# Performance work log

Measured on AMD Instinct MI355X. Metric: run time of the kernel, lower is better.

## Reference

```python
import jax, jax.numpy as jnp
import numpy as np

IN_FEATURES = 8192
OUT_FEATURES = 8192
POOL_K = 16
SCALE = 2.0


def setup_inputs() -> dict:
    key = jax.random.key(0)
    k1, k2, k3 = jax.random.split(key, 3)
    B = 4096
    x = jax.random.normal(k1, (B, IN_FEATURES), dtype=jnp.float32)
    # nn.Linear default init: U(-1/sqrt(fan_in), 1/sqrt(fan_in))
    bound = 1.0 / np.sqrt(IN_FEATURES)
    W = jax.random.uniform(k2, (OUT_FEATURES, IN_FEATURES), dtype=jnp.float32, minval=-bound, maxval=bound)
    b = jax.random.uniform(k3, (OUT_FEATURES,), dtype=jnp.float32, minval=-bound, maxval=bound)
    return {"x": x, "W": W, "b": b}


def reference(x, W, b):
    # GEMM: [B, C_out]
    y = jnp.dot(x, W.T) + b
    B, C = y.shape
    # AvgPool1d over feature dim, kernel=stride=POOL_K -> [B, C/POOL_K]
    pooled = y.reshape(B, C // POOL_K, POOL_K).mean(axis=-1)
    # GELU (tanh approximation) + scale, then row-wise max -> [B]
    v = jax.nn.gelu(pooled, approximate=True) * SCALE
    return jnp.max(v, axis=-1)
```

## Files before the change

kernel.cpp:

```cpp
#include <hip/hip_runtime.h>
#include <hip/hip_bf16.h>
#include <cmath>

#define M_DIM 4096
#define N_POOL 512
#define K_DIM 8192
#define KSPLIT 8
#define K_PER (K_DIM / KSPLIT)

typedef __bf16 bf16x8 __attribute__((ext_vector_type(8)));
typedef float floatx4 __attribute__((ext_vector_type(4)));
typedef unsigned short ushort8v __attribute__((ext_vector_type(8)));

__device__ __forceinline__ unsigned short f2bf(float f) {
  unsigned int u = __float_as_uint(f);
  return (unsigned short)((u + 0x7fffu + ((u >> 16) & 1u)) >> 16);
}

__global__ void convert_f32_bf16(const float4* __restrict__ src,
                                 ushort8v* __restrict__ dst, int n8) {
  int i = blockIdx.x * blockDim.x + threadIdx.x;
  int stride = gridDim.x * blockDim.x;
  for (; i < n8; i += stride) {
    float4 a = src[2 * i], b = src[2 * i + 1];
    ushort8v o;
    o[0] = f2bf(a.x); o[1] = f2bf(a.y); o[2] = f2bf(a.z); o[3] = f2bf(a.w);
    o[4] = f2bf(b.x); o[5] = f2bf(b.y); o[6] = f2bf(b.z); o[7] = f2bf(b.w);
    dst[i] = o;
  }
}

__global__ void wpool_kernel(const float* __restrict__ W,
                             unsigned short* __restrict__ Wp) {
  int g = blockIdx.x;
  const float* base = W + (size_t)g * 16 * K_DIM;
  ushort4* out = (ushort4*)(Wp + (size_t)g * K_DIM);
  for (int c4 = threadIdx.x; c4 < K_DIM / 4; c4 += blockDim.x) {
    float4 s = {0.f, 0.f, 0.f, 0.f};
#pragma unroll
    for (int j = 0; j < 16; ++j) {
      float4 v = ((const float4*)(base + (size_t)j * K_DIM))[c4];
      s.x += v.x; s.y += v.y; s.z += v.z; s.w += v.w;
    }
    ushort4 o;
    o.x = f2bf(s.x); o.y = f2bf(s.y); o.z = f2bf(s.z); o.w = f2bf(s.w);
    out[c4] = o;
  }
}

__global__ void bias_pool(const float* __restrict__ b, float* __restrict__ bpool) {
  int g = threadIdx.x;
  float s = 0.f;
  for (int i = 0; i < 16; ++i) s += b[g * 16 + i];
  bpool[g] = s;
}

__global__ __launch_bounds__(256) void gemm_splitk(
    const unsigned short* __restrict__ xb,
    const unsigned short* __restrict__ wp,
    float* __restrict__ part)
{
  __shared__ __align__(16) unsigned short As[128 * 64];
  __shared__ __align__(16) unsigned short Bs[128 * 64];

  const int tid = threadIdx.x;
  const int L = tid & 63;
  const int w = tid >> 6;
  const int wm = w & 1, wn = w >> 1;
  const int lane15 = L & 15, quad = L >> 4;

  const int bn = blockIdx.x, bm = blockIdx.y, kz = blockIdx.z;

  const int srow = w * 32 + (L >> 3);
  const int schunk = ((L & 7) ^ ((L >> 3) & 7)) * 8;
  const unsigned short* ga = xb + (size_t)(bm * 128 + srow) * K_DIM + kz * K_PER + schunk;
  const unsigned short* gb = wp + (size_t)(bn * 128 + srow) * K_DIM + kz * K_PER + schunk;
  unsigned short* lA = As + (w * 32) * 64;
  unsigned short* lB = Bs + (w * 32) * 64;

  floatx4 acc[4][4];
#pragma unroll
  for (int t = 0; t < 4; ++t)
#pragma unroll
    for (int u = 0; u < 4; ++u) acc[t][u] = (floatx4)0.f;

  const bf16x8* Av = (const bf16x8*)As;
  const bf16x8* Bv = (const bf16x8*)Bs;

  for (int kk = 0; kk < K_PER / 64; ++kk) {
#pragma unroll
    for (int i = 0; i < 4; ++i) {
      __builtin_amdgcn_global_load_lds(
          (const __attribute__((address_space(1))) void*)(ga + (size_t)(i * 8) * K_DIM),
          (__attribute__((address_space(3))) void*)(lA + i * 8 * 64), 16, 0, 0);
    }
#pragma unroll
    for (int i = 0; i < 4; ++i) {
      __builtin_amdgcn_global_load_lds(
          (const __attribute__((address_space(1))) void*)(gb + (size_t)(i * 8) * K_DIM),
          (__attribute__((address_space(3))) void*)(lB + i * 8 * 64), 16, 0, 0);
    }
    ga += 64; gb += 64;
    __syncthreads();

#pragma unroll
    for (int ks = 0; ks < 2; ++ks) {
      bf16x8 af[4], bfr[4];
#pragma unroll
      for (int t = 0; t < 4; ++t) {
        int r = wm * 64 + t * 16 + lane15;
        af[t] = Av[r * 8 + ((ks * 4 + quad) ^ (lane15 & 7))];
      }
#pragma unroll
      for (int u = 0; u < 4; ++u) {
        int r = wn * 64 + u * 16 + lane15;
        bfr[u] = Bv[r * 8 + ((ks * 4 + quad) ^ (lane15 & 7))];
      }
#pragma unroll
      for (int t = 0; t < 4; ++t)
#pragma unroll
        for (int u = 0; u < 4; ++u)
          acc[t][u] = __builtin_amdgcn_mfma_f32_16x16x32_bf16(af[t], bfr[u],
                                                              acc[t][u], 0, 0, 0);
    }
    __syncthreads();
  }

  float* cp = part + (size_t)kz * M_DIM * N_POOL;
  const int row_base = bm * 128 + wm * 64;
  const int col_base = bn * 128 + wn * 64;
#pragma unroll
  for (int t = 0; t < 4; ++t)
#pragma unroll
    for (int u = 0; u < 4; ++u) {
      int col = col_base + u * 16 + lane15;
#pragma unroll
      for (int r = 0; r < 4; ++r) {
        int row = row_base + t * 16 + quad * 4 + r;
        cp[(size_t)row * N_POOL + col] = acc[t][u][r];
      }
    }
}

__global__ void finalize(const float* __restrict__ part,
                         const float* __restrict__ bpool,
                         float* __restrict__ out) {
  int row = blockIdx.x;
  int lane = threadIdx.x;
  float mx = -INFINITY;
#pragma unroll
  for (int j = 0; j < 8; ++j) {
    int g = lane + j * 64;
    float s = bpool[g];
#pragma unroll
    for (int kz = 0; kz < KSPLIT; ++kz)
      s += part[(size_t)kz * M_DIM * N_POOL + (size_t)row * N_POOL + g];
    float p = s * 0.0625f;
    float t = tanhf(0.7978845608028654f * (p + 0.044715f * p * p * p));
    mx = fmaxf(mx, p * (1.0f + t));
  }
#pragma unroll
  for (int s = 32; s >= 1; s >>= 1) mx = fmaxf(mx, __shfl_xor(mx, s));
  if (lane == 0) out[row] = mx;
}

extern "C" void kernel_launch(void* const* d_in, const int* in_sizes, int n_in,
                              void* d_out, int out_size, void* d_ws, size_t ws_size,
                              hipStream_t stream) {
  const float* x = (const float*)d_in[0];
  const float* W = (const float*)d_in[1];
  const float* b = (const float*)d_in[2];
  float* out = (float*)d_out;

  char* ws = (char*)d_ws;
  unsigned short* xb = (unsigned short*)ws;
  unsigned short* Wp = (unsigned short*)(ws + (size_t)67108864);
  float* part = (float*)(ws + (size_t)75497472);
  float* bpool = (float*)(ws + (size_t)142606336);

  wpool_kernel<<<N_POOL, 256, 0, stream>>>(W, Wp);
  convert_f32_bf16<<<2048, 256, 0, stream>>>((const float4*)x, (ushort8v*)xb,
                                             (M_DIM * K_DIM) / 8);
  bias_pool<<<1, 512, 0, stream>>>(b, bpool);

  dim3 grid(N_POOL / 128, M_DIM / 128, KSPLIT);
  gemm_splitk<<<grid, 256, 0, stream>>>(xb, Wp, part);

  finalize<<<M_DIM, 64, 0, stream>>>(part, bpool, out);
}
```

Measured before the change: 518.5 us.

## Halve split-K, remap GEMM blocks per XCD, fuse bias pool, vectorize finalize

```diff
diff --git a/kernel.cpp b/kernel.cpp
--- a/kernel.cpp
+++ b/kernel.cpp
@@ -5,7 +5,7 @@
 #define M_DIM 4096
 #define N_POOL 512
 #define K_DIM 8192
-#define KSPLIT 8
+#define KSPLIT 4
 #define K_PER (K_DIM / KSPLIT)
 
 typedef __bf16 bf16x8 __attribute__((ext_vector_type(8)));
@@ -18,14 +18,25 @@
 }
 
 __global__ void convert_f32_bf16(const float4* __restrict__ src,
-                                 ushort8v* __restrict__ dst, int n8) {
+                                 ushort8v* __restrict__ dst, int n8,
+                                 const float* __restrict__ b,
+                                 float* __restrict__ bpool) {
+  if (blockIdx.x == gridDim.x - 1) {
+    for (int g = threadIdx.x; g < N_POOL; g += blockDim.x) {
+      float s = 0.f;
+#pragma unroll
+      for (int i = 0; i < 16; ++i) s += b[g * 16 + i];
+      bpool[g] = s;
+    }
+    return;
+  }
   int i = blockIdx.x * blockDim.x + threadIdx.x;
-  int stride = gridDim.x * blockDim.x;
+  int stride = (gridDim.x - 1) * blockDim.x;
   for (; i < n8; i += stride) {
-    float4 a = src[2 * i], b = src[2 * i + 1];
+    float4 a = src[2 * i], c = src[2 * i + 1];
     ushort8v o;
     o[0] = f2bf(a.x); o[1] = f2bf(a.y); o[2] = f2bf(a.z); o[3] = f2bf(a.w);
-    o[4] = f2bf(b.x); o[5] = f2bf(b.y); o[6] = f2bf(b.z); o[7] = f2bf(b.w);
+    o[4] = f2bf(c.x); o[5] = f2bf(c.y); o[6] = f2bf(c.z); o[7] = f2bf(c.w);
     dst[i] = o;
   }
 }
@@ -48,13 +59,6 @@
   }
 }
 
-__global__ void bias_pool(const float* __restrict__ b, float* __restrict__ bpool) {
-  int g = threadIdx.x;
-  float s = 0.f;
-  for (int i = 0; i < 16; ++i) s += b[g * 16 + i];
-  bpool[g] = s;
-}
-
 __global__ __launch_bounds__(256) void gemm_splitk(
     const unsigned short* __restrict__ xb,
     const unsigned short* __restrict__ wp,
@@ -69,7 +73,12 @@
   const int wm = w & 1, wn = w >> 1;
   const int lane15 = L & 15, quad = L >> 4;
 
-  const int bn = blockIdx.x, bm = blockIdx.y, kz = blockIdx.z;
+  const int id = blockIdx.x;
+  const int xcd = id & 7;
+  const int c = id >> 3;
+  const int kz = xcd >> 1;
+  const int j = (c << 1) | (xcd & 1);
+  const int bn = j & 3, bm = j >> 2;
 
   const int srow = w * 32 + (L >> 3);
   const int schunk = ((L & 7) ^ ((L >> 3) & 7)) * 8;
@@ -142,25 +151,34 @@
     }
 }
 
+__device__ __forceinline__ float gelu2(float s) {
+  float p = s * 0.0625f;
+  float t = tanhf(0.7978845608028654f * (p + 0.044715f * p * p * p));
+  return p * (1.0f + t);
+}
+
 __global__ void finalize(const float* __restrict__ part,
                          const float* __restrict__ bpool,
                          float* __restrict__ out) {
-  int row = blockIdx.x;
-  int lane = threadIdx.x;
+  const int w = threadIdx.x >> 6, lane = threadIdx.x & 63;
+  const int row = blockIdx.x * 4 + w;
+  const float4* bp4 = (const float4*)bpool;
   float mx = -INFINITY;
 #pragma unroll
-  for (int j = 0; j < 8; ++j) {
-    int g = lane + j * 64;
-    float s = bpool[g];
-#pragma unroll
-    for (int kz = 0; kz < KSPLIT; ++kz)
-      s += part[(size_t)kz * M_DIM * N_POOL + (size_t)row * N_POOL + g];
-    float p = s * 0.0625f;
-    float t = tanhf(0.7978845608028654f * (p + 0.044715f * p * p * p));
-    mx = fmaxf(mx, p * (1.0f + t));
-  }
-#pragma unroll
-  for (int s = 32; s >= 1; s >>= 1) mx = fmaxf(mx, __shfl_xor(mx, s));
+  for (int j = 0; j < 2; ++j) {
+    int g4 = lane + j * 64;
+    float4 s = bp4[g4];
+#pragma unroll
+    for (int kz = 0; kz < KSPLIT; ++kz) {
+      float4 v = ((const float4*)(part + (size_t)kz * M_DIM * N_POOL +
+                                  (size_t)row * N_POOL))[g4];
+      s.x += v.x; s.y += v.y; s.z += v.z; s.w += v.w;
+    }
+    mx = fmaxf(mx, fmaxf(fmaxf(gelu2(s.x), gelu2(s.y)),
+                         fmaxf(gelu2(s.z), gelu2(s.w))));
+  }
+#pragma unroll
+  for (int sh = 32; sh >= 1; sh >>= 1) mx = fmaxf(mx, __shfl_xor(mx, sh));
   if (lane == 0) out[row] = mx;
 }
 
@@ -176,15 +194,13 @@
   unsigned short* xb = (unsigned short*)ws;
   unsigned short* Wp = (unsigned short*)(ws + (size_t)67108864);
   float* part = (float*)(ws + (size_t)75497472);
-  float* bpool = (float*)(ws + (size_t)142606336);
+  float* bpool = (float*)(ws + (size_t)109051904);
 
   wpool_kernel<<<N_POOL, 256, 0, stream>>>(W, Wp);
-  convert_f32_bf16<<<2048, 256, 0, stream>>>((const float4*)x, (ushort8v*)xb,
-                                             (M_DIM * K_DIM) / 8);
-  bias_pool<<<1, 512, 0, stream>>>(b, bpool);
-
-  dim3 grid(N_POOL / 128, M_DIM / 128, KSPLIT);
-  gemm_splitk<<<grid, 256, 0, stream>>>(xb, Wp, part);
-
-  finalize<<<M_DIM, 64, 0, stream>>>(part, bpool, out);
-}
+  convert_f32_bf16<<<2049, 256, 0, stream>>>((const float4*)x, (ushort8v*)xb,
+                                             (M_DIM * K_DIM) / 8, b, bpool);
+
+  gemm_splitk<<<512, 256, 0, stream>>>(xb, Wp, part);
+
+  finalize<<<M_DIM / 4, 256, 0, stream>>>(part, bpool, out);
+}
```

Result: faster. 496.6 us (-4.2%).
